# Kernel tuning notes

Hardware: AMD Instinct MI355X
Metric: run time of the kernel (lower is better)

## Reference

```python
import jax, jax.numpy as jnp
import numpy as np

NB = 50  # nb_steps
IN_D = 64
HID = 128
B = 256


def _cc_weights(nb):
    # Faithful port of UMNN compute_cc_weights (Clenshaw-Curtis quadrature)
    lam = np.arange(0, nb + 1).reshape(-1, 1).astype(np.float64)
    lam = np.cos((lam @ lam.T) * np.pi / nb)
    lam[:, 0] = 0.5
    lam[:, -1] = 0.5 * lam[:, -1]
    lam = lam * 2.0 / nb
    W = np.arange(0, nb + 1).reshape(-1, 1).astype(np.float64)
    W[np.arange(1, nb + 1, 2)] = 0
    W = 2.0 / (1.0 - W ** 2)
    W[0] = 1
    W[np.arange(1, nb + 1, 2)] = 0
    cc = (lam.T @ W)[:, 0].astype(np.float32)              # [nb+1]
    steps = np.cos(np.arange(0, nb + 1) * np.pi / nb).astype(np.float32)  # [nb+1]
    return jnp.asarray(cc), jnp.asarray(steps)


def setup_inputs() -> dict:
    key = jax.random.key(0)
    ks = jax.random.split(key, 16)
    d = {}
    d["x"] = jax.random.normal(ks[0], (B, 1), dtype=jnp.float32)
    d["h"] = jax.random.normal(ks[1], (B, IN_D - 1), dtype=jnp.float32)

    def lin(kw, kb, fan_in, fan_out):
        s = 1.0 / np.sqrt(fan_in)
        w = jax.random.uniform(kw, (fan_in, fan_out), jnp.float32, -s, s)
        b = jax.random.uniform(kb, (fan_out,), jnp.float32, -s, s)
        return w, b

    # Integrand MLP: in_d -> 128 -> 128 -> 1
    d["iw0"], d["ib0"] = lin(ks[2], ks[3], IN_D, HID)
    d["iw1"], d["ib1"] = lin(ks[4], ks[5], HID, HID)
    d["iw2"], d["ib2"] = lin(ks[6], ks[7], HID, 1)
    # Outer net: (in_d-1) -> 128 -> 128 -> 2
    d["nw0"], d["nb0"] = lin(ks[8], ks[9], IN_D - 1, HID)
    d["nw1"], d["nb1"] = lin(ks[10], ks[11], HID, HID)
    d["nw2"], d["nb2"] = lin(ks[12], ks[13], HID, 2)
    return d


def reference(x, h, iw0, ib0, iw1, ib1, iw2, ib2, nw0, nb0, nw1, nb1, nw2, nb2):
    cc, steps = _cc_weights(NB)  # [S1], [S1]
    S1 = NB + 1
    b = x.shape[0]

    # ----- outer quadrature: integral over t in [0, x] -----
    # t[b, i] = 0 + (x - 0) * (steps[i] + 1) / 2
    t = x[:, None, :] * (steps[None, :, None] + 1.0) / 2.0          # [B, S1, 1]

    # ----- inner UMNN: integral over s in [t, xmax], xmax = max(t) + 10 -----
    xmax = jnp.max(t) + 10.0
    s = t[:, :, None, :] + (xmax - t)[:, :, None, :] * (steps[None, None, :, None] + 1.0) / 2.0  # [B,S1,S1,1]

    hb = jnp.broadcast_to(h[:, None, None, :], (b, S1, S1, h.shape[1]))
    inp = jnp.concatenate([s, hb], axis=-1)                         # [B,S1,S1,in_d]

    # PostiveIntegrandNN: Lin-ReLU-Lin-ReLU-Lin-ELU, then + 1.0
    a = jax.nn.relu(inp @ iw0 + ib0)
    a = jax.nn.relu(a @ iw1 + ib1)
    f = jax.nn.elu(a @ iw2 + ib2) + 1.0                              # [B,S1,S1,1]

    # inner Clenshaw-Curtis reduction: z * (xT - x0) / 2
    inner = jnp.sum(f * cc[None, None, :, None], axis=2) * (xmax - t) / 2.0   # [B,S1,1]

    # outer reduction: integral from 0 to x
    outer = jnp.sum(inner * cc[None, :, None], axis=1) * x / 2.0    # [B,1]

    # outer dense net on h -> offset / scaling
    o = jax.nn.relu(h @ nw0 + nb0)
    o = jax.nn.relu(o @ nw1 + nb1)
    o = o @ nw2 + nb2                                               # [B,2]
    offset = o[:, 0:1]
    scaling = jnp.exp(o[:, 1:2])
    return scaling * outer + offset
```

## Files before the change

### kernel.cpp

```cpp
#include <hip/hip_runtime.h>
#include <math.h>

#define NBQ 50
#define S1 51
#define NPTS 2601
#define NTILES 163
#define IN_D 64
#define HID 128
#define BSZ 256
#define NCHUNK 8

typedef __bf16 bf16x8 __attribute__((ext_vector_type(8)));
typedef float  f32x4  __attribute__((ext_vector_type(4)));

#define WS_CC     0
#define WS_STEPS  64
#define WS_XMAX   128
#define WS_BASE   256
#define WS_SCAL   33024
#define WS_OFF    33280
#define WS_PART   33536
#define WS_W1BF   35840

__global__ void k_prep(const float* __restrict__ x, const float* __restrict__ h,
                       const float* __restrict__ iw0, const float* __restrict__ ib0,
                       const float* __restrict__ iw1,
                       const float* __restrict__ nw0, const float* __restrict__ nb0,
                       const float* __restrict__ nw1, const float* __restrict__ nb1,
                       const float* __restrict__ nw2, const float* __restrict__ nb2,
                       float* __restrict__ ws) {
    int blk = blockIdx.x;
    int tid = threadIdx.x;

    if (blk < 64) {
        int idx  = blk * 256 + tid;
        int e    = idx & 7;
        int lane = (idx >> 3) & 63;
        int fk   = idx >> 9;
        int kk   = fk & 3;
        int nt   = fk >> 2;
        int k = kk * 32 + (lane >> 4) * 8 + e;
        int n = nt * 16 + (lane & 15);
        __bf16* w1bf = (__bf16*)(ws + WS_W1BF);
        w1bf[idx] = (__bf16)iw1[k * HID + n];
        return;
    }

    __shared__ float s_steps[S1];
    __shared__ float s_red[4];
    __shared__ float s_h[IN_D - 1];
    __shared__ float s_o0[HID];
    __shared__ float s_part[4];

    if (blk == 64) {
        int t = tid;
        if (t < S1) {
            double st = cos((double)t * M_PI / (double)NBQ);
            s_steps[t] = (float)st;
            ws[WS_STEPS + t] = (float)st;
            double acc = 0.0;
            for (int i = 0; i <= NBQ; ++i) {
                double Wi;
                if (i == 0)       Wi = 1.0;
                else if (i & 1)   Wi = 0.0;
                else              Wi = 2.0 / (1.0 - (double)i * (double)i);
                double lam;
                if (t == 0)  lam = 0.5;
                else         lam = cos((double)i * (double)t * M_PI / (double)NBQ);
                if (t == NBQ) lam *= 0.5;
                lam *= 2.0 / (double)NBQ;
                acc += lam * Wi;
            }
            ws[WS_CC + t] = (float)acc;
        }
        __syncthreads();
        float xb = x[t];
        float m = -1e30f;
        for (int i = 0; i < S1; ++i)
            m = fmaxf(m, xb * (s_steps[i] + 1.0f) * 0.5f);
        for (int off = 32; off > 0; off >>= 1)
            m = fmaxf(m, __shfl_down(m, off));
        if ((t & 63) == 0) s_red[t >> 6] = m;
        __syncthreads();
        if (t == 0) {
            float mm = fmaxf(fmaxf(s_red[0], s_red[1]), fmaxf(s_red[2], s_red[3]));
            ws[WS_XMAX] = mm + 10.0f;
        }
        return;
    }

    int b = blk - 65;
    int n = tid;
    bool act = (n < HID);
    if (act && n < IN_D - 1) s_h[n] = h[b * (IN_D - 1) + n];
    __syncthreads();
    float o1 = 0.0f;
    if (act) {
        float accB = ib0[n];
        float acc0 = nb0[n];
        for (int d = 0; d < IN_D - 1; ++d) {
            float hv = s_h[d];
            accB = fmaf(hv, iw0[(1 + d) * HID + n], accB);
            acc0 = fmaf(hv, nw0[d * HID + n], acc0);
        }
        ws[WS_BASE + b * HID + n] = accB;
        s_o0[n] = fmaxf(acc0, 0.0f);
    }
    __syncthreads();
    if (act) {
        float acc1 = nb1[n];
        for (int m = 0; m < HID; ++m)
            acc1 = fmaf(s_o0[m], nw1[m * HID + n], acc1);
        o1 = fmaxf(acc1, 0.0f);
    }
    float p0 = act ? o1 * nw2[n * 2 + 0] : 0.0f;
    float p1 = act ? o1 * nw2[n * 2 + 1] : 0.0f;
    for (int off = 32; off > 0; off >>= 1) {
        p0 += __shfl_down(p0, off);
        p1 += __shfl_down(p1, off);
    }
    int lane = tid & 63, w = tid >> 6;
    if (lane == 0 && w < 2) { s_part[w * 2] = p0; s_part[w * 2 + 1] = p1; }
    __syncthreads();
    if (tid == 0) {
        ws[WS_OFF + b]  = s_part[0] + s_part[2] + nb2[0];
        ws[WS_SCAL + b] = expf(s_part[1] + s_part[3] + nb2[1]);
    }
}

__global__ __launch_bounds__(64, 1) void k3_mfma(
        const float* __restrict__ x,
        const float* __restrict__ iw0,
        const float* __restrict__ ib1,
        const float* __restrict__ iw2,
        const float* __restrict__ ib2,
        float* __restrict__ ws) {
    __shared__ float s_cc[S1];
    __shared__ float s_steps[S1];

    int blk  = blockIdx.x;
    int b    = blk >> 3;
    int c    = blk & 7;
    int lane = threadIdx.x;
    int col  = lane & 15;
    int g    = lane >> 4;

    if (lane < S1) { s_cc[lane] = ws[WS_CC + lane]; s_steps[lane] = ws[WS_STEPS + lane]; }
    __syncthreads();

    float xmax = ws[WS_XMAX];
    float xb   = x[b];
    float b2   = ib2[0];

    const bf16x8* w1f = (const bf16x8*)(ws + WS_W1BF);
    bf16x8 Af[8][4];
#pragma unroll
    for (int nt = 0; nt < 8; ++nt)
#pragma unroll
        for (int kk = 0; kk < 4; ++kk)
            Af[nt][kk] = w1f[(nt * 4 + kk) * 64 + lane];

    const float* basep = ws + WS_BASE + b * HID;
    f32x4 w0a[4], w0b[4], bsa[4], bsb[4];
#pragma unroll
    for (int kk = 0; kk < 4; ++kk) {
        int m0 = kk * 32 + g * 8;
        w0a[kk] = *(const f32x4*)(iw0 + m0);
        w0b[kk] = *(const f32x4*)(iw0 + m0 + 4);
        bsa[kk] = *(const f32x4*)(basep + m0);
        bsb[kk] = *(const f32x4*)(basep + m0 + 4);
    }

    f32x4 accInit[8], iw2v[8];
#pragma unroll
    for (int nt = 0; nt < 8; ++nt) {
        accInit[nt] = *(const f32x4*)(ib1 + nt * 16 + g * 4);
        iw2v[nt]    = *(const f32x4*)(iw2 + nt * 16 + g * 4);
    }

    float vsum = 0.0f;

    for (int t = c; t < NTILES; t += NCHUNK) {
        int p  = t * 16 + col;
        int pc = (p < NPTS) ? p : (NPTS - 1);
        int i  = (int)(((unsigned)pc * 10281u) >> 19);
        int j  = pc - i * 51;
        float sti = s_steps[i];
        float stj = s_steps[j];
        float ti  = xb * (sti + 1.0f) * 0.5f;
        float w   = xmax - ti;
        float s   = fmaf(w, (stj + 1.0f) * 0.5f, ti);

        f32x4 acc[8];
        {
            bf16x8 bfr;
#pragma unroll
            for (int e = 0; e < 4; ++e)
                bfr[e] = (__bf16)fmaxf(fmaf(s, w0a[0][e], bsa[0][e]), 0.0f);
#pragma unroll
            for (int e = 0; e < 4; ++e)
                bfr[4 + e] = (__bf16)fmaxf(fmaf(s, w0b[0][e], bsb[0][e]), 0.0f);
#pragma unroll
            for (int nt = 0; nt < 8; ++nt)
                acc[nt] = __builtin_amdgcn_mfma_f32_16x16x32_bf16(Af[nt][0], bfr, accInit[nt], 0, 0, 0);
        }
#pragma unroll
        for (int kk = 1; kk < 4; ++kk) {
            bf16x8 bfr;
#pragma unroll
            for (int e = 0; e < 4; ++e)
                bfr[e] = (__bf16)fmaxf(fmaf(s, w0a[kk][e], bsa[kk][e]), 0.0f);
#pragma unroll
            for (int e = 0; e < 4; ++e)
                bfr[4 + e] = (__bf16)fmaxf(fmaf(s, w0b[kk][e], bsb[kk][e]), 0.0f);
#pragma unroll
            for (int nt = 0; nt < 8; ++nt)
                acc[nt] = __builtin_amdgcn_mfma_f32_16x16x32_bf16(Af[nt][kk], bfr, acc[nt], 0, 0, 0);
        }

        float z = 0.0f;
#pragma unroll
        for (int nt = 0; nt < 8; ++nt)
#pragma unroll
            for (int q = 0; q < 4; ++q)
                z = fmaf(fmaxf(acc[nt][q], 0.0f), iw2v[nt][q], z);
        z += __shfl_xor(z, 16);
        z += __shfl_xor(z, 32);
        z += b2;
        float f   = (z > 0.0f) ? (z + 1.0f) : __expf(z);
        float val = s_cc[i] * s_cc[j] * w * f;
        vsum += (p < NPTS) ? val : 0.0f;
    }

#pragma unroll
    for (int off = 1; off < 64; off <<= 1)
        vsum += __shfl_xor(vsum, off);
    if (lane == 0)
        ws[WS_PART + blk] = vsum * 0.125f;
}

__global__ void k4_final(const float* __restrict__ x, const float* __restrict__ ws,
                         float* __restrict__ out) {
    int b = threadIdx.x;
    float sum = 0.0f;
#pragma unroll
    for (int c = 0; c < NCHUNK; ++c) sum += ws[WS_PART + b * NCHUNK + c];
    out[b] = ws[WS_SCAL + b] * sum * x[b] * 0.5f + ws[WS_OFF + b];
}

extern "C" void kernel_launch(void* const* d_in, const int* in_sizes, int n_in,
                              void* d_out, int out_size, void* d_ws, size_t ws_size,
                              hipStream_t stream) {
    const float* x   = (const float*)d_in[0];
    const float* h   = (const float*)d_in[1];
    const float* iw0 = (const float*)d_in[2];
    const float* ib0 = (const float*)d_in[3];
    const float* iw1 = (const float*)d_in[4];
    const float* ib1 = (const float*)d_in[5];
    const float* iw2 = (const float*)d_in[6];
    const float* ib2 = (const float*)d_in[7];
    const float* nw0 = (const float*)d_in[8];
    const float* nb0 = (const float*)d_in[9];
    const float* nw1 = (const float*)d_in[10];
    const float* nb1 = (const float*)d_in[11];
    const float* nw2 = (const float*)d_in[12];
    const float* nb2 = (const float*)d_in[13];
    float* ws  = (float*)d_ws;
    float* out = (float*)d_out;

    hipLaunchKernelGGL(k_prep, dim3(64 + 1 + BSZ), dim3(256), 0, stream,
                       x, h, iw0, ib0, iw1, nw0, nb0, nw1, nb1, nw2, nb2, ws);
    hipLaunchKernelGGL(k3_mfma, dim3(BSZ * NCHUNK), dim3(64), 0, stream,
                       x, iw0, ib1, iw2, ib2, ws);
    hipLaunchKernelGGL(k4_final, dim3(1), dim3(BSZ), 0, stream, x, ws, out);
}
```

Measured before the change: 57.55 us.

## Split hidden-layer MFMA tiles across two waves per block with LDS reduction

Each block now runs two waves. Each wave holds half of the W1 fragments and computes four of the eight 16-column MFMA tiles, and the partial output dot products are combined through shared memory with a barrier on every tile iteration. Per-quadrature-point values (ti, w, step half, cc*w) are also precomputed into LDS so the inner loop does less arithmetic. The aim is to halve register pressure and double the waves in flight. The cost is a __syncthreads per tile and duplicated layer-0 activation work in both waves.

```diff
diff --git a/kernel.cpp b/kernel.cpp
--- a/kernel.cpp
+++ b/kernel.cpp
@@ -128,7 +128,7 @@
     }
 }
 
-__global__ __launch_bounds__(64, 1) void k3_mfma(
+__global__ __launch_bounds__(128, 2) void k3_mfma(
         const float* __restrict__ x,
         const float* __restrict__ iw0,
         const float* __restrict__ ib1,
@@ -136,29 +136,46 @@
         const float* __restrict__ ib2,
         float* __restrict__ ws) {
     __shared__ float s_cc[S1];
-    __shared__ float s_steps[S1];
+    __shared__ float s_ti[S1];
+    __shared__ float s_w[S1];
+    __shared__ float s_sjh[S1];
+    __shared__ float s_ccw[S1];
+    __shared__ float s_z[2][16];
 
     int blk  = blockIdx.x;
     int b    = blk >> 3;
     int c    = blk & 7;
-    int lane = threadIdx.x;
+    int tid  = threadIdx.x;
+    int wave = tid >> 6;
+    int lane = tid & 63;
     int col  = lane & 15;
     int g    = lane >> 4;
-
-    if (lane < S1) { s_cc[lane] = ws[WS_CC + lane]; s_steps[lane] = ws[WS_STEPS + lane]; }
-    __syncthreads();
 
     float xmax = ws[WS_XMAX];
     float xb   = x[b];
     float b2   = ib2[0];
 
+    if (tid < S1) {
+        float st = ws[WS_STEPS + tid];
+        float cc = ws[WS_CC + tid];
+        float ti = xb * (st + 1.0f) * 0.5f;
+        float w  = xmax - ti;
+        s_cc[tid]  = cc;
+        s_ti[tid]  = ti;
+        s_w[tid]   = w;
+        s_sjh[tid] = (st + 1.0f) * 0.5f;
+        s_ccw[tid] = cc * w;
+    }
+
     const bf16x8* w1f = (const bf16x8*)(ws + WS_W1BF);
-    bf16x8 Af[8][4];
-#pragma unroll
-    for (int nt = 0; nt < 8; ++nt)
+    bf16x8 Af[4][4];
+#pragma unroll
+    for (int nt = 0; nt < 4; ++nt) {
+        int NT = wave * 4 + nt;
 #pragma unroll
         for (int kk = 0; kk < 4; ++kk)
-            Af[nt][kk] = w1f[(nt * 4 + kk) * 64 + lane];
+            Af[nt][kk] = w1f[(NT * 4 + kk) * 64 + lane];
+    }
 
     const float* basep = ws + WS_BASE + b * HID;
     f32x4 w0a[4], w0b[4], bsa[4], bsb[4];
@@ -171,72 +188,68 @@
         bsb[kk] = *(const f32x4*)(basep + m0 + 4);
     }
 
-    f32x4 accInit[8], iw2v[8];
-#pragma unroll
-    for (int nt = 0; nt < 8; ++nt) {
-        accInit[nt] = *(const f32x4*)(ib1 + nt * 16 + g * 4);
-        iw2v[nt]    = *(const f32x4*)(iw2 + nt * 16 + g * 4);
-    }
+    f32x4 accInit[4], iw2v[4];
+#pragma unroll
+    for (int nt = 0; nt < 4; ++nt) {
+        int n0 = (wave * 4 + nt) * 16 + g * 4;
+        accInit[nt] = *(const f32x4*)(ib1 + n0);
+        iw2v[nt]    = *(const f32x4*)(iw2 + n0);
+    }
+
+    __syncthreads();
 
     float vsum = 0.0f;
+    int par = 0;
 
     for (int t = c; t < NTILES; t += NCHUNK) {
         int p  = t * 16 + col;
         int pc = (p < NPTS) ? p : (NPTS - 1);
         int i  = (int)(((unsigned)pc * 10281u) >> 19);
         int j  = pc - i * 51;
-        float sti = s_steps[i];
-        float stj = s_steps[j];
-        float ti  = xb * (sti + 1.0f) * 0.5f;
-        float w   = xmax - ti;
-        float s   = fmaf(w, (stj + 1.0f) * 0.5f, ti);
-
-        f32x4 acc[8];
-        {
+        float s = fmaf(s_w[i], s_sjh[j], s_ti[i]);
+
+        f32x4 acc[4];
+#pragma unroll
+        for (int kk = 0; kk < 4; ++kk) {
             bf16x8 bfr;
 #pragma unroll
-            for (int e = 0; e < 4; ++e)
-                bfr[e] = (__bf16)fmaxf(fmaf(s, w0a[0][e], bsa[0][e]), 0.0f);
-#pragma unroll
-            for (int e = 0; e < 4; ++e)
-                bfr[4 + e] = (__bf16)fmaxf(fmaf(s, w0b[0][e], bsb[0][e]), 0.0f);
-#pragma unroll
-            for (int nt = 0; nt < 8; ++nt)
-                acc[nt] = __builtin_amdgcn_mfma_f32_16x16x32_bf16(Af[nt][0], bfr, accInit[nt], 0, 0, 0);
-        }
-#pragma unroll
-        for (int kk = 1; kk < 4; ++kk) {
-            bf16x8 bfr;
-#pragma unroll
-            for (int e = 0; e < 4; ++e)
-                bfr[e] = (__bf16)fmaxf(fmaf(s, w0a[kk][e], bsa[kk][e]), 0.0f);
-#pragma unroll
-            for (int e = 0; e < 4; ++e)
+            for (int e = 0; e < 4; ++e) {
+                bfr[e]     = (__bf16)fmaxf(fmaf(s, w0a[kk][e], bsa[kk][e]), 0.0f);
                 bfr[4 + e] = (__bf16)fmaxf(fmaf(s, w0b[kk][e], bsb[kk][e]), 0.0f);
-#pragma unroll
-            for (int nt = 0; nt < 8; ++nt)
-                acc[nt] = __builtin_amdgcn_mfma_f32_16x16x32_bf16(Af[nt][kk], bfr, acc[nt], 0, 0, 0);
+            }
+#pragma unroll
+            for (int nt = 0; nt < 4; ++nt)
+                acc[nt] = __builtin_amdgcn_mfma_f32_16x16x32_bf16(
+                    Af[nt][kk], bfr, (kk == 0) ? accInit[nt] : acc[nt], 0, 0, 0);
         }
 
         float z = 0.0f;
 #pragma unroll
-        for (int nt = 0; nt < 8; ++nt)
+        for (int nt = 0; nt < 4; ++nt)
 #pragma unroll
             for (int q = 0; q < 4; ++q)
                 z = fmaf(fmaxf(acc[nt][q], 0.0f), iw2v[nt][q], z);
         z += __shfl_xor(z, 16);
         z += __shfl_xor(z, 32);
-        z += b2;
-        float f   = (z > 0.0f) ? (z + 1.0f) : __expf(z);
-        float val = s_cc[i] * s_cc[j] * w * f;
-        vsum += (p < NPTS) ? val : 0.0f;
-    }
-
-#pragma unroll
-    for (int off = 1; off < 64; off <<= 1)
-        vsum += __shfl_xor(vsum, off);
-    if (lane == 0)
-        ws[WS_PART + blk] = vsum * 0.125f;
+
+        if (wave == 0 && g == 0) s_z[par][col] = z;
+        __syncthreads();
+        if (wave == 1) {
+            float zf = z + s_z[par][col] + b2;
+            float f  = (zf > 0.0f) ? (zf + 1.0f) : __expf(zf);
+            float val = s_ccw[i] * s_cc[j] * f;
+            vsum += (p < NPTS) ? val : 0.0f;
+        }
+        par ^= 1;
+    }
+
+    if (wave == 1) {
+#pragma unroll
+        for (int off = 1; off < 64; off <<= 1)
+            vsum += __shfl_xor(vsum, off);
+        if (lane == 0)
+            ws[WS_PART + blk] = vsum * 0.125f;
+    }
 }
 
 __global__ void k4_final(const float* __restrict__ x, const float* __restrict__ ws,
@@ -270,7 +283,7 @@
 
     hipLaunchKernelGGL(k_prep, dim3(64 + 1 + BSZ), dim3(256), 0, stream,
                        x, h, iw0, ib0, iw1, nw0, nb0, nw1, nb1, nw2, nb2, ws);
-    hipLaunchKernelGGL(k3_mfma, dim3(BSZ * NCHUNK), dim3(64), 0, stream,
+    hipLaunchKernelGGL(k3_mfma, dim3(BSZ * NCHUNK), dim3(128), 0, stream,
                        x, iw0, ib1, iw2, ib2, ws);
     hipLaunchKernelGGL(k4_final, dim3(1), dim3(BSZ), 0, stream, x, ws, out);
 }
```

After: 57.49 us. No clear change (-0.1%).

## Pack per-batch layer-0 weights/bias and output weights as bf16 pairs to cut registers

Applied to the files above, without the earlier changes.

Packs iw0 with the per-batch layer-0 base, and iw2 with ib1, into 32-bit words holding two bf16 halves. This halves the register footprint of those loop-invariant operands, and launch bounds are raised to allow two waves per SIMD. It also precomputes per-row quadrature terms (ti, w, cc*w) in shared memory and splits the final dot product into four independent accumulators. The cost is lower precision for layer-0 weights, biases and iw2, plus extra unpack ALU work in the inner loop.

```diff
diff --git a/kernel.cpp b/kernel.cpp
--- a/kernel.cpp
+++ b/kernel.cpp
@@ -12,19 +12,33 @@
 
 typedef __bf16 bf16x8 __attribute__((ext_vector_type(8)));
 typedef float  f32x4  __attribute__((ext_vector_type(4)));
+typedef unsigned int u32x4 __attribute__((ext_vector_type(4)));
 
 #define WS_CC     0
 #define WS_STEPS  64
 #define WS_XMAX   128
-#define WS_BASE   256
-#define WS_SCAL   33024
-#define WS_OFF    33280
-#define WS_PART   33536
-#define WS_W1BF   35840
+#define WS_SCAL   192
+#define WS_OFF    448
+#define WS_PART   704
+#define WS_WB     2752
+#define WS_NIW    35520
+#define WS_W1BF   35712
+
+static __device__ inline unsigned int bf16bits(float v) {
+    __bf16 t = (__bf16)v;
+    return (unsigned int)__builtin_bit_cast(unsigned short, t);
+}
+static __device__ inline float hi_f32(unsigned int u) {
+    return __builtin_bit_cast(float, u & 0xffff0000u);
+}
+static __device__ inline float lo_f32(unsigned int u) {
+    return __builtin_bit_cast(float, u << 16);
+}
 
 __global__ void k_prep(const float* __restrict__ x, const float* __restrict__ h,
                        const float* __restrict__ iw0, const float* __restrict__ ib0,
-                       const float* __restrict__ iw1,
+                       const float* __restrict__ iw1, const float* __restrict__ ib1,
+                       const float* __restrict__ iw2,
                        const float* __restrict__ nw0, const float* __restrict__ nb0,
                        const float* __restrict__ nw1, const float* __restrict__ nb1,
                        const float* __restrict__ nw2, const float* __restrict__ nb2,
@@ -54,6 +68,10 @@
 
     if (blk == 64) {
         int t = tid;
+        if (t < HID) {
+            unsigned int* niw = (unsigned int*)(ws + WS_NIW);
+            niw[t] = (bf16bits(iw2[t]) << 16) | bf16bits(ib1[t]);
+        }
         if (t < S1) {
             double st = cos((double)t * M_PI / (double)NBQ);
             s_steps[t] = (float)st;
@@ -103,7 +121,8 @@
             accB = fmaf(hv, iw0[(1 + d) * HID + n], accB);
             acc0 = fmaf(hv, nw0[d * HID + n], acc0);
         }
-        ws[WS_BASE + b * HID + n] = accB;
+        unsigned int* wb = (unsigned int*)(ws + WS_WB);
+        wb[b * HID + n] = (bf16bits(iw0[n]) << 16) | bf16bits(accB);
         s_o0[n] = fmaxf(acc0, 0.0f);
     }
     __syncthreads();
@@ -128,15 +147,15 @@
     }
 }
 
-__global__ __launch_bounds__(64, 1) void k3_mfma(
+__global__ __launch_bounds__(64, 2) void k3_mfma(
         const float* __restrict__ x,
-        const float* __restrict__ iw0,
-        const float* __restrict__ ib1,
-        const float* __restrict__ iw2,
-        const float* __restrict__ ib2,
+        const float* __restrict__ ib2p,
         float* __restrict__ ws) {
     __shared__ float s_cc[S1];
-    __shared__ float s_steps[S1];
+    __shared__ float s_ti[S1];
+    __shared__ float s_w[S1];
+    __shared__ float s_sjh[S1];
+    __shared__ float s_ccw[S1];
 
     int blk  = blockIdx.x;
     int b    = blk >> 3;
@@ -145,12 +164,21 @@
     int col  = lane & 15;
     int g    = lane >> 4;
 
-    if (lane < S1) { s_cc[lane] = ws[WS_CC + lane]; s_steps[lane] = ws[WS_STEPS + lane]; }
-    __syncthreads();
-
     float xmax = ws[WS_XMAX];
     float xb   = x[b];
-    float b2   = ib2[0];
+    float b2   = ib2p[0];
+
+    if (lane < S1) {
+        float st = ws[WS_STEPS + lane];
+        float cc = ws[WS_CC + lane];
+        float ti = xb * (st + 1.0f) * 0.5f;
+        float w  = xmax - ti;
+        s_cc[lane]  = cc;
+        s_ti[lane]  = ti;
+        s_w[lane]   = w;
+        s_sjh[lane] = (st + 1.0f) * 0.5f;
+        s_ccw[lane] = cc * w;
+    }
 
     const bf16x8* w1f = (const bf16x8*)(ws + WS_W1BF);
     bf16x8 Af[8][4];
@@ -160,23 +188,22 @@
         for (int kk = 0; kk < 4; ++kk)
             Af[nt][kk] = w1f[(nt * 4 + kk) * 64 + lane];
 
-    const float* basep = ws + WS_BASE + b * HID;
-    f32x4 w0a[4], w0b[4], bsa[4], bsb[4];
+    const unsigned int* wbp = (const unsigned int*)(ws + WS_WB) + b * HID;
+    u32x4 wbA[4], wbB[4];
 #pragma unroll
     for (int kk = 0; kk < 4; ++kk) {
         int m0 = kk * 32 + g * 8;
-        w0a[kk] = *(const f32x4*)(iw0 + m0);
-        w0b[kk] = *(const f32x4*)(iw0 + m0 + 4);
-        bsa[kk] = *(const f32x4*)(basep + m0);
-        bsb[kk] = *(const f32x4*)(basep + m0 + 4);
-    }
-
-    f32x4 accInit[8], iw2v[8];
-#pragma unroll
-    for (int nt = 0; nt < 8; ++nt) {
-        accInit[nt] = *(const f32x4*)(ib1 + nt * 16 + g * 4);
-        iw2v[nt]    = *(const f32x4*)(iw2 + nt * 16 + g * 4);
-    }
+        wbA[kk] = *(const u32x4*)(wbp + m0);
+        wbB[kk] = *(const u32x4*)(wbp + m0 + 4);
+    }
+
+    const unsigned int* niw = (const unsigned int*)(ws + WS_NIW);
+    u32x4 nv[8];
+#pragma unroll
+    for (int nt = 0; nt < 8; ++nt)
+        nv[nt] = *(const u32x4*)(niw + nt * 16 + g * 4);
+
+    __syncthreads();
 
     float vsum = 0.0f;
 
@@ -185,50 +212,51 @@
         int pc = (p < NPTS) ? p : (NPTS - 1);
         int i  = (int)(((unsigned)pc * 10281u) >> 19);
         int j  = pc - i * 51;
-        float sti = s_steps[i];
-        float stj = s_steps[j];
-        float ti  = xb * (sti + 1.0f) * 0.5f;
-        float w   = xmax - ti;
-        float s   = fmaf(w, (stj + 1.0f) * 0.5f, ti);
+        float s = fmaf(s_w[i], s_sjh[j], s_ti[i]);
 
         f32x4 acc[8];
-        {
+#pragma unroll
+        for (int nt = 0; nt < 8; ++nt)
+#pragma unroll
+            for (int q = 0; q < 4; ++q)
+                acc[nt][q] = lo_f32(nv[nt][q]);
+
+#pragma unroll
+        for (int kk = 0; kk < 4; ++kk) {
             bf16x8 bfr;
 #pragma unroll
-            for (int e = 0; e < 4; ++e)
-                bfr[e] = (__bf16)fmaxf(fmaf(s, w0a[0][e], bsa[0][e]), 0.0f);
-#pragma unroll
-            for (int e = 0; e < 4; ++e)
-                bfr[4 + e] = (__bf16)fmaxf(fmaf(s, w0b[0][e], bsb[0][e]), 0.0f);
+            for (int e = 0; e < 4; ++e) {
+                unsigned int ua = wbA[kk][e];
+                unsigned int ub = wbB[kk][e];
+                bfr[e]     = (__bf16)fmaxf(fmaf(s, hi_f32(ua), lo_f32(ua)), 0.0f);
+                bfr[4 + e] = (__bf16)fmaxf(fmaf(s, hi_f32(ub), lo_f32(ub)), 0.0f);
+            }
 #pragma unroll
             for (int nt = 0; nt < 8; ++nt)
-                acc[nt] = __builtin_amdgcn_mfma_f32_16x16x32_bf16(Af[nt][0], bfr, accInit[nt], 0, 0, 0);
-        }
-#pragma unroll
-        for (int kk = 1; kk < 4; ++kk) {
-            bf16x8 bfr;
-#pragma unroll
-            for (int e = 0; e < 4; ++e)
-                bfr[e] = (__bf16)fmaxf(fmaf(s, w0a[kk][e], bsa[kk][e]), 0.0f);
-#pragma unroll
-            for (int e = 0; e < 4; ++e)
-                bfr[4 + e] = (__bf16)fmaxf(fmaf(s, w0b[kk][e], bsb[kk][e]), 0.0f);
-#pragma unroll
-            for (int nt = 0; nt < 8; ++nt)
-                acc[nt] = __builtin_amdgcn_mfma_f32_16x16x32_bf16(Af[nt][kk], bfr, acc[nt], 0, 0, 0);
-        }
-
-        float z = 0.0f;
-#pragma unroll
-        for (int nt = 0; nt < 8; ++nt)
-#pragma unroll
-            for (int q = 0; q < 4; ++q)
-                z = fmaf(fmaxf(acc[nt][q], 0.0f), iw2v[nt][q], z);
+                acc[nt] = __builtin_amdgcn_mfma_f32_16x16x32_bf16(
+                    Af[nt][kk], bfr, acc[nt], 0, 0, 0);
+        }
+
+        float z0 = 0.f, z1 = 0.f, z2 = 0.f, z3 = 0.f;
+#pragma unroll
+        for (int nt = 0; nt < 8; ++nt) {
+#pragma unroll
+            for (int q = 0; q < 4; ++q) {
+                float iw2f = hi_f32(nv[nt][q]);
+                float v = fmaxf(acc[nt][q], 0.0f);
+                if (q == 0)      z0 = fmaf(v, iw2f, z0);
+                else if (q == 1) z1 = fmaf(v, iw2f, z1);
+                else if (q == 2) z2 = fmaf(v, iw2f, z2);
+                else             z3 = fmaf(v, iw2f, z3);
+            }
+        }
+        float z = (z0 + z1) + (z2 + z3);
         z += __shfl_xor(z, 16);
         z += __shfl_xor(z, 32);
         z += b2;
-        float f   = (z > 0.0f) ? (z + 1.0f) : __expf(z);
-        float val = s_cc[i] * s_cc[j] * w * f;
+        float ez = __expf(fminf(z, 0.0f));
+        float f  = (z > 0.0f) ? (z + 1.0f) : ez;
+        float val = s_ccw[i] * s_cc[j] * f;
         vsum += (p < NPTS) ? val : 0.0f;
     }
 
@@ -269,8 +297,8 @@
     float* out = (float*)d_out;
 
     hipLaunchKernelGGL(k_prep, dim3(64 + 1 + BSZ), dim3(256), 0, stream,
-                       x, h, iw0, ib0, iw1, nw0, nb0, nw1, nb1, nw2, nb2, ws);
+                       x, h, iw0, ib0, iw1, ib1, iw2, nw0, nb0, nw1, nb1, nw2, nb2, ws);
     hipLaunchKernelGGL(k3_mfma, dim3(BSZ * NCHUNK), dim3(64), 0, stream,
-                       x, iw0, ib1, iw2, ib2, ws);
+                       x, ib2, ws);
     hipLaunchKernelGGL(k4_final, dim3(1), dim3(BSZ), 0, stream, x, ws, out);
 }
```

After: 83.82 us. +45.6%, slower.

## Defer per-tile epilogue to LDS batch pass and precompute quadrature tables

Applied to the files above, without the earlier changes.

Each tile's partial output dot product is now written to an LDS buffer, and the cross-group reduction, ELU and quadrature weighting run in one pass after the MFMA loop. This takes the shuffles, exp and weight lookups off the per-tile critical path. Per-i quadrature values (t, xmax-t, cc*w) and the per-j step factor are precomputed into shared memory. The next tile's s value is computed ahead of the MFMAs. The cost is extra LDS and a changed accumulation scaling, because each point is now counted once instead of four times.

```diff
diff --git a/kernel.cpp b/kernel.cpp
--- a/kernel.cpp
+++ b/kernel.cpp
@@ -9,6 +9,7 @@
 #define HID 128
 #define BSZ 256
 #define NCHUNK 8
+#define NUMAX 21
 
 typedef __bf16 bf16x8 __attribute__((ext_vector_type(8)));
 typedef float  f32x4  __attribute__((ext_vector_type(4)));
@@ -136,7 +137,11 @@
         const float* __restrict__ ib2,
         float* __restrict__ ws) {
     __shared__ float s_cc[S1];
-    __shared__ float s_steps[S1];
+    __shared__ float s_ti[S1];
+    __shared__ float s_w[S1];
+    __shared__ float s_sjh[S1];
+    __shared__ float s_ccw[S1];
+    __shared__ float zlds[NUMAX][68];
 
     int blk  = blockIdx.x;
     int b    = blk >> 3;
@@ -145,12 +150,21 @@
     int col  = lane & 15;
     int g    = lane >> 4;
 
-    if (lane < S1) { s_cc[lane] = ws[WS_CC + lane]; s_steps[lane] = ws[WS_STEPS + lane]; }
-    __syncthreads();
-
     float xmax = ws[WS_XMAX];
     float xb   = x[b];
     float b2   = ib2[0];
+
+    if (lane < S1) {
+        float st = ws[WS_STEPS + lane];
+        float cc = ws[WS_CC + lane];
+        float ti = xb * (st + 1.0f) * 0.5f;
+        float w  = xmax - ti;
+        s_cc[lane]  = cc;
+        s_ti[lane]  = ti;
+        s_w[lane]   = w;
+        s_sjh[lane] = (st + 1.0f) * 0.5f;
+        s_ccw[lane] = cc * w;
+    }
 
     const bf16x8* w1f = (const bf16x8*)(ws + WS_W1BF);
     bf16x8 Af[8][4];
@@ -178,65 +192,80 @@
         iw2v[nt]    = *(const f32x4*)(iw2 + nt * 16 + g * 4);
     }
 
+    __syncthreads();
+
+    int NU = (c <= 2) ? 21 : 20;
+
+    {
+    }
+    int pc0 = c * 16 + col;
+    if (pc0 >= NPTS) pc0 = NPTS - 1;
+    int i_c = (int)(((unsigned)pc0 * 10281u) >> 19);
+    int j_c = pc0 - i_c * 51;
+    float s_cur = fmaf(s_w[i_c], s_sjh[j_c], s_ti[i_c]);
+
+    for (int u = 0; u < NU; ++u) {
+        bf16x8 bfr[4];
+#pragma unroll
+        for (int kk = 0; kk < 4; ++kk) {
+#pragma unroll
+            for (int e = 0; e < 4; ++e) {
+                bfr[kk][e]     = (__bf16)fmaxf(fmaf(s_cur, w0a[kk][e], bsa[kk][e]), 0.0f);
+                bfr[kk][4 + e] = (__bf16)fmaxf(fmaf(s_cur, w0b[kk][e], bsb[kk][e]), 0.0f);
+            }
+        }
+
+        int t2 = c + 8 * (u + 1);
+        int pc2 = t2 * 16 + col;
+        if (pc2 >= NPTS) pc2 = NPTS - 1;
+        int i_n = (int)(((unsigned)pc2 * 10281u) >> 19);
+        int j_n = pc2 - i_n * 51;
+        float s_nxt = fmaf(s_w[i_n], s_sjh[j_n], s_ti[i_n]);
+
+        f32x4 acc[8];
+#pragma unroll
+        for (int kk = 0; kk < 4; ++kk)
+#pragma unroll
+            for (int nt = 0; nt < 8; ++nt)
+                acc[nt] = __builtin_amdgcn_mfma_f32_16x16x32_bf16(
+                    Af[nt][kk], bfr[kk], (kk == 0) ? accInit[nt] : acc[nt], 0, 0, 0);
+
+        float z0 = 0.f, z1 = 0.f, z2 = 0.f, z3 = 0.f;
+#pragma unroll
+        for (int nt = 0; nt < 8; ++nt) {
+            z0 = fmaf(fmaxf(acc[nt][0], 0.0f), iw2v[nt][0], z0);
+            z1 = fmaf(fmaxf(acc[nt][1], 0.0f), iw2v[nt][1], z1);
+            z2 = fmaf(fmaxf(acc[nt][2], 0.0f), iw2v[nt][2], z2);
+            z3 = fmaf(fmaxf(acc[nt][3], 0.0f), iw2v[nt][3], z3);
+        }
+        zlds[u][g * 16 + col] = (z0 + z1) + (z2 + z3);
+
+        s_cur = s_nxt;
+    }
+
     float vsum = 0.0f;
-
-    for (int t = c; t < NTILES; t += NCHUNK) {
-        int p  = t * 16 + col;
-        int pc = (p < NPTS) ? p : (NPTS - 1);
-        int i  = (int)(((unsigned)pc * 10281u) >> 19);
-        int j  = pc - i * 51;
-        float sti = s_steps[i];
-        float stj = s_steps[j];
-        float ti  = xb * (sti + 1.0f) * 0.5f;
-        float w   = xmax - ti;
-        float s   = fmaf(w, (stj + 1.0f) * 0.5f, ti);
-
-        f32x4 acc[8];
-        {
-            bf16x8 bfr;
-#pragma unroll
-            for (int e = 0; e < 4; ++e)
-                bfr[e] = (__bf16)fmaxf(fmaf(s, w0a[0][e], bsa[0][e]), 0.0f);
-#pragma unroll
-            for (int e = 0; e < 4; ++e)
-                bfr[4 + e] = (__bf16)fmaxf(fmaf(s, w0b[0][e], bsb[0][e]), 0.0f);
-#pragma unroll
-            for (int nt = 0; nt < 8; ++nt)
-                acc[nt] = __builtin_amdgcn_mfma_f32_16x16x32_bf16(Af[nt][0], bfr, accInit[nt], 0, 0, 0);
-        }
-#pragma unroll
-        for (int kk = 1; kk < 4; ++kk) {
-            bf16x8 bfr;
-#pragma unroll
-            for (int e = 0; e < 4; ++e)
-                bfr[e] = (__bf16)fmaxf(fmaf(s, w0a[kk][e], bsa[kk][e]), 0.0f);
-#pragma unroll
-            for (int e = 0; e < 4; ++e)
-                bfr[4 + e] = (__bf16)fmaxf(fmaf(s, w0b[kk][e], bsb[kk][e]), 0.0f);
-#pragma unroll
-            for (int nt = 0; nt < 8; ++nt)
-                acc[nt] = __builtin_amdgcn_mfma_f32_16x16x32_bf16(Af[nt][kk], bfr, acc[nt], 0, 0, 0);
-        }
-
-        float z = 0.0f;
-#pragma unroll
-        for (int nt = 0; nt < 8; ++nt)
-#pragma unroll
-            for (int q = 0; q < 4; ++q)
-                z = fmaf(fmaxf(acc[nt][q], 0.0f), iw2v[nt][q], z);
-        z += __shfl_xor(z, 16);
-        z += __shfl_xor(z, 32);
-        z += b2;
-        float f   = (z > 0.0f) ? (z + 1.0f) : __expf(z);
-        float val = s_cc[i] * s_cc[j] * w * f;
-        vsum += (p < NPTS) ? val : 0.0f;
+    int npass = (NU + 3) >> 2;
+    for (int pass = 0; pass < npass; ++pass) {
+        int u = pass * 4 + g;
+        if (u < NU) {
+            int t = c + 8 * u;
+            int p = t * 16 + col;
+            if (p < NPTS) {
+                float z = zlds[u][col] + zlds[u][16 + col]
+                        + zlds[u][32 + col] + zlds[u][48 + col] + b2;
+                float f = (z > 0.0f) ? (z + 1.0f) : __expf(z);
+                int i = (int)(((unsigned)p * 10281u) >> 19);
+                int j = p - i * 51;
+                vsum += s_ccw[i] * s_cc[j] * f;
+            }
+        }
     }
 
 #pragma unroll
     for (int off = 1; off < 64; off <<= 1)
         vsum += __shfl_xor(vsum, off);
     if (lane == 0)
-        ws[WS_PART + blk] = vsum * 0.125f;
+        ws[WS_PART + blk] = vsum * 0.5f;
 }
 
 __global__ void k4_final(const float* __restrict__ x, const float* __restrict__ ws,
```

New measurement: 51.16 us. 1.12x faster.
